# Performance work log

Hardware: AMD Instinct MI355X
Metric: run time of the kernel (lower is better)

## Reference

```python
import jax, jax.numpy as jnp
import numpy as np

R = 16
ALPHA = 32.0
SCALING = ALPHA / R


def setup_inputs() -> dict:
    key = jax.random.key(0)
    ks = jax.random.split(key, 6)
    B, T, C, O, E = 16, 1500, 1024, 1024, 8
    x = jax.random.normal(ks[0], (B, T, C), dtype=jnp.float32)
    # gate weights per batch element (e.g. softmax-like, but module accepts any)
    w = jax.random.uniform(ks[1], (B, E), dtype=jnp.float32)
    W_base = jax.random.normal(ks[2], (O, C), dtype=jnp.float32) * 0.02
    b_base = jax.random.normal(ks[3], (O,), dtype=jnp.float32) * 0.02
    As = jax.random.normal(ks[4], (E, R, C), dtype=jnp.float32) * 0.02
    Bs = jax.random.normal(ks[5], (E, O, R), dtype=jnp.float32) * 0.02
    return {"x": x, "w": w, "W_base": W_base, "b_base": b_base, "As": As, "Bs": Bs}


def reference(x, w, W_base, b_base, As, Bs):
    # base linear: (B,T,C) @ (C,O) + b
    out = jnp.einsum('btc,oc->bto', x, W_base) + b_base
    # per-expert low-rank: h[b,t,e,r] = x[b,t,:] @ A_e^T
    h = jnp.einsum('btc,erc->bter', x, As)          # (B,T,E,R)
    # y[b,t,e,o] = h @ B_e^T ; gate-weighted sum over experts
    lora = jnp.einsum('bter,eor,be->bto', h, Bs, w)  # (B,T,O)
    return out + lora * SCALING
```

## Files before the change

kernel.cpp:

```cpp
#include <hip/hip_runtime.h>
#include <stdint.h>
#include <stddef.h>


#define B_ 16
#define T_ 1500
#define C_ 1024
#define O_ 1024
#define E_ 8
#define R_ 16
#define SCALING 2.0f

typedef __bf16 bf16x8 __attribute__((ext_vector_type(8)));
typedef float f32x4 __attribute__((ext_vector_type(4)));
typedef unsigned short u16;

__device__ inline u16 f2bf(float f) {
  union { float f; unsigned u; } v; v.f = f;
  unsigned u = v.u;
  u += 0x7fff + ((u >> 16) & 1);
  return (u16)(u >> 16);
}

__global__ __launch_bounds__(256) void cvt_x(const float4* __restrict__ x,
                                             ushort4* __restrict__ xb) {
  int i = blockIdx.x * 256 + threadIdx.x;
  float4 v = x[i];
  ushort4 o;
  o.x = f2bf(v.x); o.y = f2bf(v.y); o.z = f2bf(v.z); o.w = f2bf(v.w);
  xb[i] = o;
}

__global__ __launch_bounds__(256) void build_wm(const float* __restrict__ w,
                                                const float* __restrict__ Wb,
                                                const float* __restrict__ As,
                                                const float* __restrict__ Bs,
                                                u16* __restrict__ wm) {
  int idx = blockIdx.x * 256 + threadIdx.x;
  int o = idx >> 10;
  int c = idx & 1023;
  float d[E_];
#pragma unroll
  for (int e = 0; e < E_; ++e) {
    float acc = 0.f;
#pragma unroll
    for (int r = 0; r < R_; ++r)
      acc += Bs[(e * O_ + o) * R_ + r] * As[(e * R_ + r) * C_ + c];
    d[e] = acc;
  }
  float base = Wb[idx];
#pragma unroll
  for (int b = 0; b < B_; ++b) {
    float s = 0.f;
#pragma unroll
    for (int e = 0; e < E_; ++e) s += w[b * E_ + e] * d[e];
    wm[(size_t)b * (O_ * C_) + idx] = f2bf(base + SCALING * s);
  }
}

__global__ __launch_bounds__(256) void gemm_merged(const u16* __restrict__ xb,
                                                   const u16* __restrict__ wm,
                                                   const float* __restrict__ bbase,
                                                   float* __restrict__ out) {
  const int mt = blockIdx.x;
  const int nt = blockIdx.y;
  const int b = blockIdx.z;
  const int tid = threadIdx.x;
  const int lane = tid & 63;
  const int wv = tid >> 6;
  const int wrow = wv & 1;
  const int wcol = wv >> 1;
  const int l15 = lane & 15;
  const int quad = lane >> 4;

  __shared__ u16 lA[128 * 32];
  __shared__ u16 lB[128 * 32];

  const u16* gA = xb + ((size_t)b * T_ + (size_t)mt * 128) * C_;
  const u16* gB = wm + ((size_t)b * O_ + (size_t)nt * 128) * C_;

  f32x4 acc[4][4];
#pragma unroll
  for (int i = 0; i < 4; ++i)
#pragma unroll
    for (int j = 0; j < 4; ++j) acc[i][j] = (f32x4){0.f, 0.f, 0.f, 0.f};

  const int idx0 = tid;
  const int idx1 = 256 + tid;
  const int r0 = idx0 >> 2, kc0 = idx0 & 3;
  const int r1 = idx1 >> 2, kc1 = idx1 & 3;

  for (int kt = 0; kt < C_ / 32; ++kt) {
    const int k0 = kt * 32;
    __builtin_amdgcn_global_load_lds(
        (const __attribute__((address_space(1))) void*)(gA + (size_t)r0 * C_ + k0 + kc0 * 8),
        (__attribute__((address_space(3))) void*)(&lA[idx0 * 8]), 16, 0, 0);
    __builtin_amdgcn_global_load_lds(
        (const __attribute__((address_space(1))) void*)(gA + (size_t)r1 * C_ + k0 + kc1 * 8),
        (__attribute__((address_space(3))) void*)(&lA[idx1 * 8]), 16, 0, 0);
    __builtin_amdgcn_global_load_lds(
        (const __attribute__((address_space(1))) void*)(gB + (size_t)r0 * C_ + k0 + kc0 * 8),
        (__attribute__((address_space(3))) void*)(&lB[idx0 * 8]), 16, 0, 0);
    __builtin_amdgcn_global_load_lds(
        (const __attribute__((address_space(1))) void*)(gB + (size_t)r1 * C_ + k0 + kc1 * 8),
        (__attribute__((address_space(3))) void*)(&lB[idx1 * 8]), 16, 0, 0);
    __syncthreads();

    bf16x8 af[4], bfr[4];
#pragma unroll
    for (int i = 0; i < 4; ++i) {
      af[i] = *(const bf16x8*)&lA[(wrow * 64 + i * 16 + l15) * 32 + quad * 8];
      bfr[i] = *(const bf16x8*)&lB[(wcol * 64 + i * 16 + l15) * 32 + quad * 8];
    }
#pragma unroll
    for (int i = 0; i < 4; ++i)
#pragma unroll
      for (int j = 0; j < 4; ++j)
        acc[i][j] = __builtin_amdgcn_mfma_f32_16x16x32_bf16(af[i], bfr[j], acc[i][j], 0, 0, 0);
    __syncthreads();
  }

#pragma unroll
  for (int j = 0; j < 4; ++j) {
    const int col = nt * 128 + wcol * 64 + j * 16 + l15;
    const float bias = bbase[col];
#pragma unroll
    for (int i = 0; i < 4; ++i) {
#pragma unroll
      for (int r = 0; r < 4; ++r) {
        const int row = mt * 128 + wrow * 64 + i * 16 + quad * 4 + r;
        if (row < T_) out[((size_t)b * T_ + row) * O_ + col] = acc[i][j][r] + bias;
      }
    }
  }
}

extern "C" void kernel_launch(void* const* d_in, const int* in_sizes, int n_in,
                              void* d_out, int out_size, void* d_ws, size_t ws_size,
                              hipStream_t stream) {
  const float* x = (const float*)d_in[0];
  const float* w = (const float*)d_in[1];
  const float* Wb = (const float*)d_in[2];
  const float* bb = (const float*)d_in[3];
  const float* As = (const float*)d_in[4];
  const float* Bs = (const float*)d_in[5];
  float* out = (float*)d_out;

  u16* xb = (u16*)d_ws;
  u16* wmp = xb + (size_t)B_ * T_ * C_;

  cvt_x<<<24000, 256, 0, stream>>>((const float4*)x, (ushort4*)xb);
  build_wm<<<4096, 256, 0, stream>>>(w, Wb, As, Bs, wmp);
  gemm_merged<<<dim3(12, 8, 16), 256, 0, stream>>>(xb, wmp, bb, out);
}
```

Measured before the change: 306.2 us.

## Replace per-batch merged weights with concatenated LoRA K-extension GEMM

Instead of building sixteen per-batch merged weight matrices, the LoRA branch becomes a small h=x·A^T GEMM whose gate-scaled output is appended as extra K columns of x. A single shared weight [W_base | B_e] with K=1152 then lets one flat GEMM over all B*T rows cover both base and LoRA terms. This removes the large per-batch weight build and its memory traffic, and lets the main GEMM reuse one weight matrix across batches, at the cost of an extra kernel and a larger K. It also adds an XOR swizzle on the LDS layout to reduce bank conflicts, and linearizes the grid so tiles sharing rows of x run close together.

After: 310.3 us. Within noise of the previous version (+1.3%).

```diff
diff --git a/kernel.cpp b/kernel.cpp
--- a/kernel.cpp
+++ b/kernel.cpp
@@ -9,6 +9,9 @@
 #define O_ 1024
 #define E_ 8
 #define R_ 16
+#define ER 128
+#define KK 1152
+#define BT 24000
 #define SCALING 2.0f
 
 typedef __bf16 bf16x8 __attribute__((ext_vector_type(8)));
@@ -22,62 +25,56 @@
   return (u16)(u >> 16);
 }
 
+#define GLL(gp, lp)                                                            \
+  __builtin_amdgcn_global_load_lds(                                            \
+      (const __attribute__((address_space(1))) void*)(gp),                     \
+      (__attribute__((address_space(3))) void*)(lp), 16, 0, 0)
+
 __global__ __launch_bounds__(256) void cvt_x(const float4* __restrict__ x,
-                                             ushort4* __restrict__ xb) {
+                                             u16* __restrict__ xp) {
   int i = blockIdx.x * 256 + threadIdx.x;
   float4 v = x[i];
+  int row = i >> 8;
+  int c = (i & 255) << 2;
   ushort4 o;
   o.x = f2bf(v.x); o.y = f2bf(v.y); o.z = f2bf(v.z); o.w = f2bf(v.w);
-  xb[i] = o;
-}
-
-__global__ __launch_bounds__(256) void build_wm(const float* __restrict__ w,
-                                                const float* __restrict__ Wb,
-                                                const float* __restrict__ As,
-                                                const float* __restrict__ Bs,
-                                                u16* __restrict__ wm) {
+  *(ushort4*)(xp + (size_t)row * KK + c) = o;
+}
+
+__global__ __launch_bounds__(256) void prep_w(const float* __restrict__ Wb,
+                                              const float* __restrict__ Bs,
+                                              const float* __restrict__ As,
+                                              u16* __restrict__ wp,
+                                              u16* __restrict__ ap) {
   int idx = blockIdx.x * 256 + threadIdx.x;
-  int o = idx >> 10;
-  int c = idx & 1023;
-  float d[E_];
-#pragma unroll
-  for (int e = 0; e < E_; ++e) {
-    float acc = 0.f;
-#pragma unroll
-    for (int r = 0; r < R_; ++r)
-      acc += Bs[(e * O_ + o) * R_ + r] * As[(e * R_ + r) * C_ + c];
-    d[e] = acc;
-  }
-  float base = Wb[idx];
-#pragma unroll
-  for (int b = 0; b < B_; ++b) {
-    float s = 0.f;
-#pragma unroll
-    for (int e = 0; e < E_; ++e) s += w[b * E_ + e] * d[e];
-    wm[(size_t)b * (O_ * C_) + idx] = f2bf(base + SCALING * s);
-  }
-}
-
-__global__ __launch_bounds__(256) void gemm_merged(const u16* __restrict__ xb,
-                                                   const u16* __restrict__ wm,
-                                                   const float* __restrict__ bbase,
-                                                   float* __restrict__ out) {
+  if (idx < O_ * KK) {
+    int o = idx / KK;
+    int k = idx - o * KK;
+    float v;
+    if (k < C_) {
+      v = Wb[o * C_ + k];
+    } else {
+      int j = k - C_;
+      v = Bs[((j >> 4) * O_ + o) * R_ + (j & 15)];
+    }
+    wp[idx] = f2bf(v);
+  } else {
+    int a = idx - O_ * KK;
+    ap[a] = f2bf(As[a]);
+  }
+}
+
+__global__ __launch_bounds__(256) void h_gemm(u16* __restrict__ xp,
+                                              const u16* __restrict__ ab,
+                                              const float* __restrict__ w) {
   const int mt = blockIdx.x;
-  const int nt = blockIdx.y;
-  const int b = blockIdx.z;
-  const int tid = threadIdx.x;
-  const int lane = tid & 63;
-  const int wv = tid >> 6;
-  const int wrow = wv & 1;
-  const int wcol = wv >> 1;
-  const int l15 = lane & 15;
-  const int quad = lane >> 4;
+  const int tid = threadIdx.x, lane = tid & 63, wv = tid >> 6;
+  const int wrow = wv & 1, wcol = wv >> 1, l15 = lane & 15, quad = lane >> 4;
+  const int kx = quad ^ (l15 & 3) ^ ((l15 >> 2) & 3);
 
   __shared__ u16 lA[128 * 32];
   __shared__ u16 lB[128 * 32];
-
-  const u16* gA = xb + ((size_t)b * T_ + (size_t)mt * 128) * C_;
-  const u16* gB = wm + ((size_t)b * O_ + (size_t)nt * 128) * C_;
+  const u16* gA = xp + (size_t)mt * 128 * KK;
 
   f32x4 acc[4][4];
 #pragma unroll
@@ -85,32 +82,22 @@
 #pragma unroll
     for (int j = 0; j < 4; ++j) acc[i][j] = (f32x4){0.f, 0.f, 0.f, 0.f};
 
-  const int idx0 = tid;
-  const int idx1 = 256 + tid;
-  const int r0 = idx0 >> 2, kc0 = idx0 & 3;
-  const int r1 = idx1 >> 2, kc1 = idx1 & 3;
+  const int idx0 = tid, idx1 = 256 + tid;
+  const int r0 = idx0 >> 2, kc0 = (idx0 & 3) ^ (r0 & 3) ^ ((r0 >> 2) & 3);
+  const int r1 = idx1 >> 2, kc1 = (idx1 & 3) ^ (r1 & 3) ^ ((r1 >> 2) & 3);
 
   for (int kt = 0; kt < C_ / 32; ++kt) {
     const int k0 = kt * 32;
-    __builtin_amdgcn_global_load_lds(
-        (const __attribute__((address_space(1))) void*)(gA + (size_t)r0 * C_ + k0 + kc0 * 8),
-        (__attribute__((address_space(3))) void*)(&lA[idx0 * 8]), 16, 0, 0);
-    __builtin_amdgcn_global_load_lds(
-        (const __attribute__((address_space(1))) void*)(gA + (size_t)r1 * C_ + k0 + kc1 * 8),
-        (__attribute__((address_space(3))) void*)(&lA[idx1 * 8]), 16, 0, 0);
-    __builtin_amdgcn_global_load_lds(
-        (const __attribute__((address_space(1))) void*)(gB + (size_t)r0 * C_ + k0 + kc0 * 8),
-        (__attribute__((address_space(3))) void*)(&lB[idx0 * 8]), 16, 0, 0);
-    __builtin_amdgcn_global_load_lds(
-        (const __attribute__((address_space(1))) void*)(gB + (size_t)r1 * C_ + k0 + kc1 * 8),
-        (__attribute__((address_space(3))) void*)(&lB[idx1 * 8]), 16, 0, 0);
-    __syncthreads();
-
+    GLL(gA + (size_t)r0 * KK + k0 + kc0 * 8, &lA[idx0 * 8]);
+    GLL(gA + (size_t)r1 * KK + k0 + kc1 * 8, &lA[idx1 * 8]);
+    GLL(ab + r0 * C_ + k0 + kc0 * 8, &lB[idx0 * 8]);
+    GLL(ab + r1 * C_ + k0 + kc1 * 8, &lB[idx1 * 8]);
+    __syncthreads();
     bf16x8 af[4], bfr[4];
 #pragma unroll
     for (int i = 0; i < 4; ++i) {
-      af[i] = *(const bf16x8*)&lA[(wrow * 64 + i * 16 + l15) * 32 + quad * 8];
-      bfr[i] = *(const bf16x8*)&lB[(wcol * 64 + i * 16 + l15) * 32 + quad * 8];
+      af[i] = *(const bf16x8*)&lA[(wrow * 64 + i * 16 + l15) * 32 + kx * 8];
+      bfr[i] = *(const bf16x8*)&lB[(wcol * 64 + i * 16 + l15) * 32 + kx * 8];
     }
 #pragma unroll
     for (int i = 0; i < 4; ++i)
@@ -122,14 +109,79 @@
 
 #pragma unroll
   for (int j = 0; j < 4; ++j) {
+    const int col = wcol * 64 + j * 16 + l15;
+    const int e = wcol * 4 + j;
+#pragma unroll
+    for (int i = 0; i < 4; ++i) {
+#pragma unroll
+      for (int rr = 0; rr < 4; ++rr) {
+        const int row = mt * 128 + wrow * 64 + i * 16 + quad * 4 + rr;
+        if (row < BT) {
+          const int b = row / T_;
+          xp[(size_t)row * KK + C_ + col] = f2bf(acc[i][j][rr] * (SCALING * w[b * E_ + e]));
+        }
+      }
+    }
+  }
+}
+
+__global__ __launch_bounds__(256) void main_gemm(const u16* __restrict__ xp,
+                                                 const u16* __restrict__ wp,
+                                                 const float* __restrict__ bb,
+                                                 float* __restrict__ out) {
+  const int id = blockIdx.x;
+  const int nt = id & 7;
+  const int mt = id >> 3;
+  const int tid = threadIdx.x, lane = tid & 63, wv = tid >> 6;
+  const int wrow = wv & 1, wcol = wv >> 1, l15 = lane & 15, quad = lane >> 4;
+  const int kx = quad ^ (l15 & 3) ^ ((l15 >> 2) & 3);
+
+  __shared__ u16 lA[128 * 32];
+  __shared__ u16 lB[128 * 32];
+  const u16* gA = xp + (size_t)mt * 128 * KK;
+  const u16* gB = wp + (size_t)nt * 128 * KK;
+
+  f32x4 acc[4][4];
+#pragma unroll
+  for (int i = 0; i < 4; ++i)
+#pragma unroll
+    for (int j = 0; j < 4; ++j) acc[i][j] = (f32x4){0.f, 0.f, 0.f, 0.f};
+
+  const int idx0 = tid, idx1 = 256 + tid;
+  const int r0 = idx0 >> 2, kc0 = (idx0 & 3) ^ (r0 & 3) ^ ((r0 >> 2) & 3);
+  const int r1 = idx1 >> 2, kc1 = (idx1 & 3) ^ (r1 & 3) ^ ((r1 >> 2) & 3);
+
+  for (int kt = 0; kt < KK / 32; ++kt) {
+    const int k0 = kt * 32;
+    GLL(gA + (size_t)r0 * KK + k0 + kc0 * 8, &lA[idx0 * 8]);
+    GLL(gA + (size_t)r1 * KK + k0 + kc1 * 8, &lA[idx1 * 8]);
+    GLL(gB + (size_t)r0 * KK + k0 + kc0 * 8, &lB[idx0 * 8]);
+    GLL(gB + (size_t)r1 * KK + k0 + kc1 * 8, &lB[idx1 * 8]);
+    __syncthreads();
+    bf16x8 af[4], bfr[4];
+#pragma unroll
+    for (int i = 0; i < 4; ++i) {
+      af[i] = *(const bf16x8*)&lA[(wrow * 64 + i * 16 + l15) * 32 + kx * 8];
+      bfr[i] = *(const bf16x8*)&lB[(wcol * 64 + i * 16 + l15) * 32 + kx * 8];
+    }
+#pragma unroll
+    for (int i = 0; i < 4; ++i)
+#pragma unroll
+      for (int j = 0; j < 4; ++j)
+        acc[i][j] = __builtin_amdgcn_mfma_f32_16x16x32_bf16(af[i], bfr[j], acc[i][j], 0, 0, 0);
+    __syncthreads();
+  }
+
+#pragma unroll
+  for (int j = 0; j < 4; ++j) {
     const int col = nt * 128 + wcol * 64 + j * 16 + l15;
-    const float bias = bbase[col];
-#pragma unroll
-    for (int i = 0; i < 4; ++i) {
-#pragma unroll
-      for (int r = 0; r < 4; ++r) {
-        const int row = mt * 128 + wrow * 64 + i * 16 + quad * 4 + r;
-        if (row < T_) out[((size_t)b * T_ + row) * O_ + col] = acc[i][j][r] + bias;
+    const float bias = bb[col];
+#pragma unroll
+    for (int i = 0; i < 4; ++i) {
+#pragma unroll
+      for (int rr = 0; rr < 4; ++rr) {
+        const int row = mt * 128 + wrow * 64 + i * 16 + quad * 4 + rr;
+        if (row < BT) out[(size_t)row * O_ + col] = acc[i][j][rr] + bias;
       }
     }
   }
@@ -146,10 +198,12 @@
   const float* Bs = (const float*)d_in[5];
   float* out = (float*)d_out;
 
-  u16* xb = (u16*)d_ws;
-  u16* wmp = xb + (size_t)B_ * T_ * C_;
-
-  cvt_x<<<24000, 256, 0, stream>>>((const float4*)x, (ushort4*)xb);
-  build_wm<<<4096, 256, 0, stream>>>(w, Wb, As, Bs, wmp);
-  gemm_merged<<<dim3(12, 8, 16), 256, 0, stream>>>(xb, wmp, bb, out);
-}
+  u16* xp = (u16*)d_ws;
+  u16* wp = xp + (size_t)BT * KK;
+  u16* ap = wp + (size_t)O_ * KK;
+
+  prep_w<<<(O_ * KK + ER * C_) / 256, 256, 0, stream>>>(Wb, Bs, As, wp, ap);
+  cvt_x<<<BT * C_ / 1024, 256, 0, stream>>>((const float4*)x, xp);
+  h_gemm<<<188, 256, 0, stream>>>(xp, ap, w);
+  main_gemm<<<1504, 256, 0, stream>>>(xp, wp, bb, out);
+}
```
